# Optimization experiments

Hardware: AMD Instinct MI355X
Metric: run time of the kernel (lower is better)

The kernel has to match this reference:

```python
import jax, jax.numpy as jnp
import numpy as np

NBIT = 8
NSPLIT = 255.0  # 2**NBIT - 1


def _quantized_matmul(x, w_clean, eps):
    # Faithful port of quantization(): bit-slice x into NBIT binary planes, run a
    # noisy linear per plane with weight w + randn*|w|*0.1, and sum. The 8
    # sequential fc() calls are fused into one einsum over the bit axis.
    # x: (..., in); w_clean: (out, in); eps: (NBIT, out, in) standard normal.
    mn = jnp.min(x)
    mx = jnp.max(x)
    q = ((x - mn) / (mx - mn) * NSPLIT).astype(jnp.uint8).astype(jnp.int32)  # truncating cast as in torch
    quant_base = 2 ** jnp.arange(NBIT, dtype=jnp.int32)
    binary = ((q[..., None] & quant_base) != 0).astype(x.dtype)              # (..., in, NBIT)
    scaled = binary * (2.0 ** jnp.arange(NBIT)).astype(x.dtype)              # plane i scaled by 2**i
    w_noisy = w_clean[None] + eps * jnp.abs(w_clean)[None] * 0.1             # (NBIT, out, in)
    z = jnp.einsum('...ib,boi->...o', scaled, w_noisy)
    return z, mn, mx, w_noisy[-1]  # fc.weight after loop == last noisy weight


def _forward(node_embedding, edge_embedding, nbr_mask, cond1, cond2, eps1, eps2, bn_gamma, bn_beta):
    B, At, Nbr, Fe = edge_embedding.shape
    Fn = node_embedding.shape[-1]
    c1 = jnp.concatenate(
        [jnp.broadcast_to(node_embedding[:, :, None, :], (B, At, Nbr, Fn)), edge_embedding],
        axis=3)                                                              # (B, At, Nbr, Fn+Fe)
    # quantization + re_quantization through fc (re-quant uses last noisy fc.weight)
    z1, mn1, mx1, w_last = _quantized_matmul(c1, cond1[0], eps1)
    bias1 = jnp.sum(mn1 * w_last, axis=1)                                    # (H1,)
    h = jax.nn.relu(z1 / NSPLIT * (mx1 - mn1) + bias1)                       # (B, At, Nbr, H1)
    # quantization + re_quantization through fc_2 (re-quant uses conductance[1][-1])
    z2, mn2, mx2, _ = _quantized_matmul(h, cond2[0], eps2)
    bias2 = jnp.sum(mn2 * cond2[-1], axis=1)                                 # (2*Fn,)
    c2 = z2 / NSPLIT * (mx2 - mn2) + bias2                                   # (B, At, Nbr, 2*Fn)
    nbr_gate, nbr_extract = jnp.split(c2, 2, axis=3)
    nbr_sumed = jax.nn.sigmoid(nbr_gate) * jnp.tanh(nbr_extract) * nbr_mask[..., None]
    nbr_sumed = jnp.sum(nbr_sumed, axis=2)                                   # (B, At, Fn)
    # BatchNorm1d in training mode: batch statistics over flattened (B*At)
    flat = nbr_sumed.reshape(-1, Fn)
    mean = jnp.mean(flat, axis=0)
    var = jnp.var(flat, axis=0)  # biased variance, as torch BN uses for normalization
    bn = ((flat - mean) / jnp.sqrt(var + 1e-5) * bn_gamma + bn_beta).reshape(B, At, Fn)
    return jax.nn.relu(node_embedding + bn)


def setup_inputs() -> dict:
    key = jax.random.key(0)
    ks = jax.random.split(key, 7)
    B, At, Nbr, Fn, Fe = 16, 96, 12, 64, 64
    H1, H2 = 4 * (Fn + Fe), 2 * Fn
    return {
        'node_embedding': jax.random.normal(ks[0], (B, At, Fn), jnp.float32),
        'edge_embedding': jax.random.normal(ks[1], (B, At, Nbr, Fe), jnp.float32),
        'nbr_mask': (jax.random.uniform(ks[2], (B, At, Nbr)) > 0.5).astype(jnp.float32),
        'cond1': jax.random.normal(ks[3], (2, H1, Fn + Fe), jnp.float32) * 0.05,
        'cond2': jax.random.normal(ks[4], (2, H2, H1), jnp.float32) * 0.05,
        'eps1': jax.random.normal(ks[5], (NBIT, H1, Fn + Fe), jnp.float32),
        'eps2': jax.random.normal(ks[6], (NBIT, H2, H1), jnp.float32),
        'bn_gamma': jnp.ones((Fn,), jnp.float32),
        'bn_beta': jnp.zeros((Fn,), jnp.float32),
    }


def reference(node_embedding, edge_embedding, nbr_mask, cond1, cond2, eps1, eps2, bn_gamma, bn_beta):
    return _forward(node_embedding, edge_embedding, nbr_mask, cond1, cond2, eps1, eps2, bn_gamma, bn_beta)
```

## Files before the change

kernel.cpp:

```cpp
#include <hip/hip_runtime.h>
#include <stdint.h>

#define B_    16
#define AT_   96
#define NBR_  12
#define FN_   64
#define FE_   64
#define M1    (B_*AT_*NBR_)
#define R_    (B_*AT_)
#define K1Q   128
#define N1    512
#define K2Q   512
#define N2    128
#define SPLIT2 4

typedef _Float16 f16x8 __attribute__((ext_vector_type(8)));
typedef float    f32x4 __attribute__((ext_vector_type(4)));
typedef __attribute__((address_space(1))) const void gconst_void;
typedef __attribute__((address_space(3))) void lds_void;

#define OFF_SCAL  0u
#define OFF_Q1    256u
#define OFF_W1E   (OFF_Q1  + (size_t)M1*K1Q)
#define OFF_B1    (OFF_W1E + (size_t)N1*K1Q*8*2)
#define OFF_B2    (OFF_B1  + (size_t)N1*4)
#define OFF_W2E   (OFF_B2  + (size_t)N2*4 + 256)
#define OFF_Q2    (OFF_W2E + (size_t)N2*K2Q*8*2)
#define OFF_H     (OFF_Q2  + (size_t)M1*K2Q)
#define OFF_ZP    OFF_H
#define OFF_NS    (OFF_H   + (size_t)M1*N1*4)

__device__ __forceinline__ unsigned int enc_f(float f) {
    unsigned int u = __float_as_uint(f);
    return (u & 0x80000000u) ? ~u : (u | 0x80000000u);
}
__device__ __forceinline__ float dec_f(unsigned int u) {
    return __uint_as_float((u & 0x80000000u) ? (u & 0x7FFFFFFFu) : ~u);
}

__global__ void k_init(unsigned int* scal) {
    if (threadIdx.x == 0) {
        scal[0] = 0xFFFFFFFFu; scal[1] = 0u;
        scal[2] = 0xFFFFFFFFu; scal[3] = 0u;
    }
}

__global__ __launch_bounds__(256) void k_minmax_c1(const float* __restrict__ node,
                                                   const float* __restrict__ edge,
                                                   unsigned int* __restrict__ scal) {
    const int nn = B_*AT_*FN_;
    const int ntot = nn + M1*FE_;
    float mn = 3.0e38f, mx = -3.0e38f;
    for (int idx = blockIdx.x*blockDim.x + threadIdx.x; idx < ntot; idx += gridDim.x*blockDim.x) {
        float x = (idx < nn) ? node[idx] : edge[idx - nn];
        mn = fminf(mn, x); mx = fmaxf(mx, x);
    }
    __shared__ float smn[256], smx[256];
    smn[threadIdx.x] = mn; smx[threadIdx.x] = mx; __syncthreads();
    for (int s = 128; s > 0; s >>= 1) {
        if (threadIdx.x < s) {
            smn[threadIdx.x] = fminf(smn[threadIdx.x], smn[threadIdx.x+s]);
            smx[threadIdx.x] = fmaxf(smx[threadIdx.x], smx[threadIdx.x+s]);
        }
        __syncthreads();
    }
    if (threadIdx.x == 0) { atomicMin(&scal[0], enc_f(smn[0])); atomicMax(&scal[1], enc_f(smx[0])); }
}

template<int KQ, int N>
__global__ __launch_bounds__(256) void k_prep_w16(const float* __restrict__ w_clean,
                                                  const float* __restrict__ eps,
                                                  const unsigned int* __restrict__ scal, int sbase,
                                                  _Float16* __restrict__ We) {
    int idx = blockIdx.x*blockDim.x + threadIdx.x;
    if (idx >= N*KQ) return;
    int o = idx / KQ, i = idx % KQ;
    float mn = dec_f(scal[sbase]), mx = dec_f(scal[sbase+1]);
    float s = (mx - mn) * (1.0f/255.0f);
    float w = w_clean[idx];
    float aw = fabsf(w) * 0.1f;
    union { _Float16 h[8]; uint4 u; } pk;
    float p = s;
    #pragma unroll
    for (int b = 0; b < 8; b++) {
        float e = eps[(size_t)b*N*KQ + idx];
        pk.h[b] = (_Float16)((w + e*aw) * p);
        p *= 2.0f;
    }
    *(uint4*)&We[((size_t)o*KQ + i)*8] = pk.u;
}

__global__ void k_bias1(const float* __restrict__ cond1, const float* __restrict__ eps1,
                        const unsigned int* __restrict__ scal, float* __restrict__ bias1) {
    int o = blockIdx.x*blockDim.x + threadIdx.x;
    if (o >= N1) return;
    float mn = dec_f(scal[0]);
    float ssum = 0.f;
    for (int i = 0; i < K1Q; i++) {
        float w = cond1[o*K1Q + i];
        float e = eps1[7*(N1*K1Q) + o*K1Q + i];
        ssum += w + (e * fabsf(w)) * 0.1f;
    }
    bias1[o] = mn * ssum;
}

__global__ void k_bias2(const float* __restrict__ cond2, const unsigned int* __restrict__ scal,
                        float* __restrict__ bias2) {
    int o = blockIdx.x*blockDim.x + threadIdx.x;
    if (o >= N2) return;
    float mn = dec_f(scal[2]);
    const float* w2 = cond2 + N2*K2Q;
    float ssum = 0.f;
    for (int i = 0; i < K2Q; i++) ssum += w2[o*K2Q + i];
    bias2[o] = mn * ssum;
}

__global__ __launch_bounds__(256) void k_quant_c1(const float* __restrict__ node,
                                                  const float* __restrict__ edge,
                                                  const unsigned int* __restrict__ scal,
                                                  unsigned int* __restrict__ q1) {
    int idx = blockIdx.x*256 + threadIdx.x;
    int m = idx >> 5, dw = idx & 31;
    const float mn = dec_f(scal[0]), rng = dec_f(scal[1]) - mn;
    float4 x;
    if (dw < 16) x = *(const float4*)&node[(m/NBR_)*FN_ + dw*4];
    else         x = *(const float4*)&edge[(size_t)m*FE_ + (dw-16)*4];
    unsigned int b0 = (unsigned char)(int)((x.x - mn) / rng * 255.0f);
    unsigned int b1 = (unsigned char)(int)((x.y - mn) / rng * 255.0f);
    unsigned int b2 = (unsigned char)(int)((x.z - mn) / rng * 255.0f);
    unsigned int b3 = (unsigned char)(int)((x.w - mn) / rng * 255.0f);
    q1[idx] = b0 | (b1 << 8) | (b2 << 16) | (b3 << 24);
}

__global__ __launch_bounds__(256) void k_quant_h(const float* __restrict__ h,
                                                 const unsigned int* __restrict__ scal,
                                                 unsigned int* __restrict__ q2) {
    int idx = blockIdx.x*256 + threadIdx.x;
    const float mn = dec_f(scal[2]), rng = dec_f(scal[3]) - mn;
    float4 x = *(const float4*)&h[(size_t)idx*4];
    unsigned int b0 = (unsigned char)(int)((x.x - mn) / rng * 255.0f);
    unsigned int b1 = (unsigned char)(int)((x.y - mn) / rng * 255.0f);
    unsigned int b2 = (unsigned char)(int)((x.z - mn) / rng * 255.0f);
    unsigned int b3 = (unsigned char)(int)((x.w - mn) / rng * 255.0f);
    q2[idx] = b0 | (b1 << 8) | (b2 << 16) | (b3 << 24);
}

__device__ __forceinline__ f16x8 expand_byte(unsigned int byte) {
    unsigned int r2 = byte | (byte << 15);
    union { unsigned int u[4]; f16x8 h; } t;
    t.u[0] = ( r2       & 0x00010001u) * 0x3C00u;
    t.u[1] = ((r2 >> 2) & 0x00010001u) * 0x3C00u;
    t.u[2] = ((r2 >> 4) & 0x00010001u) * 0x3C00u;
    t.u[3] = ((r2 >> 6) & 0x00010001u) * 0x3C00u;
    return t.h;
}

template<int KQ, int N, int SPLITK, bool EPI1>
__global__ __launch_bounds__(256, 2) void k_gemm16(const unsigned char* __restrict__ q,
                                                   const _Float16* __restrict__ W,
                                                   const float* __restrict__ bias,
                                                   float* __restrict__ out,
                                                   unsigned int* __restrict__ scal) {
    constexpr int KP  = KQ * 8;
    constexpr int KPS = KP / SPLITK;
    __shared__ _Float16 Bs[128*64];
    __shared__ unsigned int Qs[256];

    const int tid  = threadIdx.x;
    const int lane = tid & 63;
    const int w    = tid >> 6;
    const int wm   = (w & 1) * 64;
    const int wn   = (w >> 1) * 64;
    const int l15  = lane & 15;
    const int lq   = lane >> 4;
    const int sh8  = lq * 8;
    const int m0   = blockIdx.x * 128;
    const int o0   = blockIdx.y * 128;
    const int kbase = blockIdx.z * KPS;

    f32x4 acc[4][4] = {};

    const size_t qrow = (size_t)(m0 + (tid >> 1)) * KQ + (tid & 1) * 4;

    #pragma unroll 1
    for (int it = 0; it < KPS/64; ++it) {
        const int kp0 = kbase + it*64;
        const int i0  = kp0 >> 3;
        __syncthreads();
        {
            unsigned int qa = *(const unsigned int*)(q + qrow + i0);
            #pragma unroll
            for (int iss = 0; iss < 4; ++iss) {
                int s   = iss*256 + tid;
                int n   = s >> 3;
                int csrc = (s & 7) ^ (n & 7);
                const _Float16* gp = W + (size_t)(o0 + n)*KP + kp0 + csrc*8;
                _Float16* lp = &Bs[(size_t)(iss*256 + (tid & ~63)) * 8];
                __builtin_amdgcn_global_load_lds((gconst_void*)gp, (lds_void*)lp, 16, 0, 0);
            }
            Qs[tid] = qa;
        }
        __builtin_amdgcn_s_waitcnt(0);
        __syncthreads();

        f16x8 bf[4][2];
        #pragma unroll
        for (int nf = 0; nf < 4; ++nf) {
            const int nl = wn + nf*16 + l15;
            #pragma unroll
            for (int kf = 0; kf < 2; ++kf) {
                const int ch = kf*4 + lq;
                bf[nf][kf] = *(const f16x8*)&Bs[nl*64 + ((ch ^ (nl & 7)) << 3)];
            }
        }
        #pragma unroll
        for (int mf = 0; mf < 4; ++mf) {
            uint2 qd = *(const uint2*)&Qs[(wm + mf*16 + l15) * 2];
            f16x8 a0 = expand_byte((qd.x >> sh8) & 0xFFu);
            f16x8 a1 = expand_byte((qd.y >> sh8) & 0xFFu);
            #pragma unroll
            for (int nf = 0; nf < 4; ++nf) {
                acc[mf][nf] = __builtin_amdgcn_mfma_f32_16x16x32_f16(a0, bf[nf][0], acc[mf][nf], 0, 0, 0);
                acc[mf][nf] = __builtin_amdgcn_mfma_f32_16x16x32_f16(a1, bf[nf][1], acc[mf][nf], 0, 0, 0);
            }
        }
    }

    if (EPI1) {
        float bv[4];
        #pragma unroll
        for (int nf = 0; nf < 4; ++nf) bv[nf] = bias[o0 + wn + nf*16 + l15];
        float tmn = 3.0e38f, tmx = -3.0e38f;
        #pragma unroll
        for (int mf = 0; mf < 4; ++mf) {
            const int mr = m0 + wm + mf*16 + lq*4;
            #pragma unroll
            for (int nf = 0; nf < 4; ++nf) {
                const int oc = o0 + wn + nf*16 + l15;
                #pragma unroll
                for (int r = 0; r < 4; ++r) {
                    float v = acc[mf][nf][r] + bv[nf];
                    v = fmaxf(v, 0.0f);
                    tmn = fminf(tmn, v); tmx = fmaxf(tmx, v);
                    out[(size_t)(mr + r)*N + oc] = v;
                }
            }
        }
        __syncthreads();
        float* red = (float*)Bs;
        red[tid] = tmn; red[256 + tid] = tmx;
        __syncthreads();
        for (int s = 128; s > 0; s >>= 1) {
            if (tid < s) {
                red[tid]       = fminf(red[tid],       red[tid + s]);
                red[256 + tid] = fmaxf(red[256 + tid], red[256 + tid + s]);
            }
            __syncthreads();
        }
        if (tid == 0) { atomicMin(&scal[2], enc_f(red[0])); atomicMax(&scal[3], enc_f(red[256])); }
    } else {
        float* op = out + (size_t)blockIdx.z * ((size_t)M1 * N);
        #pragma unroll
        for (int mf = 0; mf < 4; ++mf) {
            const int mr = m0 + wm + mf*16 + lq*4;
            #pragma unroll
            for (int nf = 0; nf < 4; ++nf) {
                const int oc = o0 + wn + nf*16 + l15;
                #pragma unroll
                for (int r = 0; r < 4; ++r)
                    op[(size_t)(mr + r)*N + oc] = acc[mf][nf][r];
            }
        }
    }
}

__global__ void k_nbr(const float* __restrict__ zp, const float* __restrict__ bias2,
                      const float* __restrict__ mask, float* __restrict__ ns) {
    const size_t SP = (size_t)M1 * N2;
    int r = blockIdx.x;
    int f = threadIdx.x;
    float bg = bias2[f], be = bias2[64 + f];
    float s = 0.f;
    #pragma unroll
    for (int n = 0; n < NBR_; n++) {
        int m = r*NBR_ + n;
        size_t base = (size_t)m * N2;
        float g = bg, e = be;
        #pragma unroll
        for (int z = 0; z < SPLIT2; z++) {
            g += zp[z*SP + base + f];
            e += zp[z*SP + base + 64 + f];
        }
        float sig = 1.0f / (1.0f + expf(-g));
        s += sig * tanhf(e) * mask[m];
    }
    ns[r*64 + f] = s;
}

__global__ __launch_bounds__(256) void k_bn(const float* __restrict__ ns,
                                            const float* __restrict__ node,
                                            const float* __restrict__ gamma,
                                            const float* __restrict__ beta,
                                            float* __restrict__ out) {
    int f = blockIdx.x;
    int tid = threadIdx.x;
    float x[6];
    float s = 0.f, ss = 0.f;
    #pragma unroll
    for (int k = 0; k < 6; k++) {
        int r = tid + k*256;
        x[k] = ns[r*64 + f];
        s += x[k]; ss += x[k]*x[k];
    }
    __shared__ float rs[256], rss[256];
    rs[tid] = s; rss[tid] = ss; __syncthreads();
    for (int st = 128; st > 0; st >>= 1) {
        if (tid < st) { rs[tid] += rs[tid+st]; rss[tid] += rss[tid+st]; }
        __syncthreads();
    }
    float mean = rs[0] / 1536.0f;
    float var  = rss[0] / 1536.0f - mean*mean;
    float denom = sqrtf(var + 1e-5f);
    float g = gamma[f], bt = beta[f];
    #pragma unroll
    for (int k = 0; k < 6; k++) {
        int r = tid + k*256;
        float v = node[r*64 + f] + ((x[k] - mean) / denom * g + bt);
        out[r*64 + f] = fmaxf(v, 0.f);
    }
}

extern "C" void kernel_launch(void* const* d_in, const int* in_sizes, int n_in,
                              void* d_out, int out_size, void* d_ws, size_t ws_size,
                              hipStream_t stream) {
    const float* node  = (const float*)d_in[0];
    const float* edge  = (const float*)d_in[1];
    const float* mask  = (const float*)d_in[2];
    const float* cond1 = (const float*)d_in[3];
    const float* cond2 = (const float*)d_in[4];
    const float* eps1  = (const float*)d_in[5];
    const float* eps2  = (const float*)d_in[6];
    const float* gamma = (const float*)d_in[7];
    const float* beta  = (const float*)d_in[8];
    float* out = (float*)d_out;
    char* ws = (char*)d_ws;

    unsigned int*  scal = (unsigned int*)(ws + OFF_SCAL);
    unsigned char* q1   = (unsigned char*)(ws + OFF_Q1);
    _Float16* W1e = (_Float16*)(ws + OFF_W1E);
    float*    b1  = (float*)(ws + OFF_B1);
    float*    b2  = (float*)(ws + OFF_B2);
    _Float16* W2e = (_Float16*)(ws + OFF_W2E);
    unsigned char* q2 = (unsigned char*)(ws + OFF_Q2);
    float* h  = (float*)(ws + OFF_H);
    float* zp = (float*)(ws + OFF_ZP);
    float* ns = (float*)(ws + OFF_NS);

    k_init<<<1, 64, 0, stream>>>(scal);
    k_minmax_c1<<<512, 256, 0, stream>>>(node, edge, scal);
    k_prep_w16<K1Q, N1><<<(N1*K1Q + 255)/256, 256, 0, stream>>>(cond1, eps1, scal, 0, W1e);
    k_bias1<<<(N1 + 63)/64, 64, 0, stream>>>(cond1, eps1, scal, b1);
    k_quant_c1<<<(M1*32)/256, 256, 0, stream>>>(node, edge, scal, (unsigned int*)q1);
    k_gemm16<K1Q, N1, 1, true><<<dim3(M1/128, N1/128, 1), 256, 0, stream>>>(q1, W1e, b1, h, scal);
    k_prep_w16<K2Q, N2><<<(N2*K2Q + 255)/256, 256, 0, stream>>>(cond2, eps2, scal, 2, W2e);
    k_bias2<<<(N2 + 63)/64, 64, 0, stream>>>(cond2, scal, b2);
    k_quant_h<<<(M1*128)/256, 256, 0, stream>>>(h, scal, (unsigned int*)q2);
    k_gemm16<K2Q, N2, SPLIT2, false><<<dim3(M1/128, N2/128, SPLIT2), 256, 0, stream>>>(q2, W2e, (const float*)nullptr, zp, scal);
    k_nbr<<<R_, 64, 0, stream>>>(zp, b2, mask, ns);
    k_bn<<<64, 256, 0, stream>>>(ns, node, gamma, beta, out);
}
```

Measured before the change: 212.1 us.

## Split GEMM tile along K across warps, fuse bias into weight prep, fp16 partials

```diff
diff --git a/kernel.cpp b/kernel.cpp
--- a/kernel.cpp
+++ b/kernel.cpp
@@ -20,11 +20,11 @@
 typedef __attribute__((address_space(3))) void lds_void;
 
 #define OFF_SCAL  0u
-#define OFF_Q1    256u
+#define OFF_B1R   256u
+#define OFF_B2R   (OFF_B1R + 2048u)
+#define OFF_Q1    4096u
 #define OFF_W1E   (OFF_Q1  + (size_t)M1*K1Q)
-#define OFF_B1    (OFF_W1E + (size_t)N1*K1Q*8*2)
-#define OFF_B2    (OFF_B1  + (size_t)N1*4)
-#define OFF_W2E   (OFF_B2  + (size_t)N2*4 + 256)
+#define OFF_W2E   (OFF_W1E + (size_t)N1*K1Q*8*2)
 #define OFF_Q2    (OFF_W2E + (size_t)N2*K2Q*8*2)
 #define OFF_H     (OFF_Q2  + (size_t)M1*K2Q)
 #define OFF_ZP    OFF_H
@@ -38,11 +38,11 @@
     return __uint_as_float((u & 0x80000000u) ? (u & 0x7FFFFFFFu) : ~u);
 }
 
-__global__ void k_init(unsigned int* scal) {
-    if (threadIdx.x == 0) {
-        scal[0] = 0xFFFFFFFFu; scal[1] = 0u;
-        scal[2] = 0xFFFFFFFFu; scal[3] = 0u;
-    }
+__global__ void k_init(unsigned int* scal, float* b1raw, float* b2raw) {
+    int t = threadIdx.x;
+    if (t == 0) { scal[0] = 0xFFFFFFFFu; scal[1] = 0u; scal[2] = 0xFFFFFFFFu; scal[3] = 0u; }
+    if (t < N1) b1raw[t] = 0.f;
+    if (t < N2) b2raw[t] = 0.f;
 }
 
 __global__ __launch_bounds__(256) void k_minmax_c1(const float* __restrict__ node,
@@ -67,52 +67,36 @@
     if (threadIdx.x == 0) { atomicMin(&scal[0], enc_f(smn[0])); atomicMax(&scal[1], enc_f(smx[0])); }
 }
 
-template<int KQ, int N>
+template<int KQ, int N, int SBASE, bool USE_SECOND>
 __global__ __launch_bounds__(256) void k_prep_w16(const float* __restrict__ w_clean,
                                                   const float* __restrict__ eps,
-                                                  const unsigned int* __restrict__ scal, int sbase,
+                                                  const unsigned int* __restrict__ scal,
+                                                  float* __restrict__ braw,
                                                   _Float16* __restrict__ We) {
     int idx = blockIdx.x*blockDim.x + threadIdx.x;
     if (idx >= N*KQ) return;
-    int o = idx / KQ, i = idx % KQ;
-    float mn = dec_f(scal[sbase]), mx = dec_f(scal[sbase+1]);
+    int o = idx / KQ;
+    int i = idx % KQ;
+    float mn = dec_f(scal[SBASE]), mx = dec_f(scal[SBASE+1]);
     float s = (mx - mn) * (1.0f/255.0f);
     float w = w_clean[idx];
     float aw = fabsf(w) * 0.1f;
     union { _Float16 h[8]; uint4 u; } pk;
     float p = s;
+    float v7 = 0.f;
     #pragma unroll
     for (int b = 0; b < 8; b++) {
         float e = eps[(size_t)b*N*KQ + idx];
-        pk.h[b] = (_Float16)((w + e*aw) * p);
+        float v = w + e*aw;
+        if (b == 7) v7 = v;
+        pk.h[b] = (_Float16)(v * p);
         p *= 2.0f;
     }
     *(uint4*)&We[((size_t)o*KQ + i)*8] = pk.u;
-}
-
-__global__ void k_bias1(const float* __restrict__ cond1, const float* __restrict__ eps1,
-                        const unsigned int* __restrict__ scal, float* __restrict__ bias1) {
-    int o = blockIdx.x*blockDim.x + threadIdx.x;
-    if (o >= N1) return;
-    float mn = dec_f(scal[0]);
-    float ssum = 0.f;
-    for (int i = 0; i < K1Q; i++) {
-        float w = cond1[o*K1Q + i];
-        float e = eps1[7*(N1*K1Q) + o*K1Q + i];
-        ssum += w + (e * fabsf(w)) * 0.1f;
-    }
-    bias1[o] = mn * ssum;
-}
-
-__global__ void k_bias2(const float* __restrict__ cond2, const unsigned int* __restrict__ scal,
-                        float* __restrict__ bias2) {
-    int o = blockIdx.x*blockDim.x + threadIdx.x;
-    if (o >= N2) return;
-    float mn = dec_f(scal[2]);
-    const float* w2 = cond2 + N2*K2Q;
-    float ssum = 0.f;
-    for (int i = 0; i < K2Q; i++) ssum += w2[o*K2Q + i];
-    bias2[o] = mn * ssum;
+    float bv = USE_SECOND ? w_clean[(size_t)N*KQ + idx] : v7;
+    #pragma unroll
+    for (int off = 32; off > 0; off >>= 1) bv += __shfl_down(bv, off);
+    if ((threadIdx.x & 63) == 0) atomicAdd(&braw[o], bv);
 }
 
 __global__ __launch_bounds__(256) void k_quant_c1(const float* __restrict__ node,
@@ -156,98 +140,118 @@
 }
 
 template<int KQ, int N, int SPLITK, bool EPI1>
-__global__ __launch_bounds__(256, 2) void k_gemm16(const unsigned char* __restrict__ q,
-                                                   const _Float16* __restrict__ W,
-                                                   const float* __restrict__ bias,
-                                                   float* __restrict__ out,
-                                                   unsigned int* __restrict__ scal) {
+__global__ __launch_bounds__(256, 4) void kg(const unsigned char* __restrict__ q,
+                                             const _Float16* __restrict__ W,
+                                             const float* __restrict__ braw,
+                                             void* __restrict__ outv,
+                                             unsigned int* __restrict__ scal) {
     constexpr int KP  = KQ * 8;
     constexpr int KPS = KP / SPLITK;
-    __shared__ _Float16 Bs[128*64];
-    __shared__ unsigned int Qs[256];
+    __shared__ _Float16 Bs[8192];
+    __shared__ uint2    Qs[256];
 
     const int tid  = threadIdx.x;
     const int lane = tid & 63;
     const int w    = tid >> 6;
     const int wm   = (w & 1) * 64;
-    const int wn   = (w >> 1) * 64;
+    const int kg   = w >> 1;
     const int l15  = lane & 15;
     const int lq   = lane >> 4;
     const int sh8  = lq * 8;
     const int m0   = blockIdx.x * 128;
-    const int o0   = blockIdx.y * 128;
+    const int o0   = blockIdx.y * 64;
     const int kbase = blockIdx.z * KPS;
 
     f32x4 acc[4][4] = {};
 
-    const size_t qrow = (size_t)(m0 + (tid >> 1)) * KQ + (tid & 1) * 4;
+    const int akg = tid >> 7, agt = tid & 127;
+    const unsigned char* aq = q + (size_t)(m0 + agt)*KQ + (kbase >> 3) + akg*64;
 
     #pragma unroll 1
-    for (int it = 0; it < KPS/64; ++it) {
-        const int kp0 = kbase + it*64;
-        const int i0  = kp0 >> 3;
-        __syncthreads();
-        {
-            unsigned int qa = *(const unsigned int*)(q + qrow + i0);
-            #pragma unroll
-            for (int iss = 0; iss < 4; ++iss) {
-                int s   = iss*256 + tid;
-                int n   = s >> 3;
-                int csrc = (s & 7) ^ (n & 7);
-                const _Float16* gp = W + (size_t)(o0 + n)*KP + kp0 + csrc*8;
-                _Float16* lp = &Bs[(size_t)(iss*256 + (tid & ~63)) * 8];
-                __builtin_amdgcn_global_load_lds((gconst_void*)gp, (lds_void*)lp, 16, 0, 0);
-            }
-            Qs[tid] = qa;
-        }
+    for (int it = 0; it < KPS/128; ++it) {
+        __syncthreads();
+        uint2 qa = *(const uint2*)(aq + it*8);
+        #pragma unroll
+        for (int iss = 0; iss < 4; ++iss) {
+            int s    = iss*256 + tid;
+            int skg  = s >> 9;
+            int sg   = s & 511;
+            int n    = sg >> 3;
+            int csrc = (sg & 7) ^ (n & 7);
+            const _Float16* gp = W + (size_t)(o0 + n)*KP + kbase + skg*512 + it*64 + csrc*8;
+            _Float16* lp = &Bs[(size_t)(iss*256 + (tid & ~63)) * 8];
+            __builtin_amdgcn_global_load_lds((gconst_void*)gp, (lds_void*)lp, 16, 0, 0);
+        }
+        Qs[(akg << 7) + agt] = qa;
         __builtin_amdgcn_s_waitcnt(0);
         __syncthreads();
 
-        f16x8 bf[4][2];
+        uint2 qd[4];
         #pragma unroll
-        for (int nf = 0; nf < 4; ++nf) {
-            const int nl = wn + nf*16 + l15;
-            #pragma unroll
-            for (int kf = 0; kf < 2; ++kf) {
+        for (int mf = 0; mf < 4; ++mf)
+            qd[mf] = Qs[kg*128 + wm + mf*16 + l15];
+        #pragma unroll
+        for (int kf = 0; kf < 2; ++kf) {
+            f16x8 bf[4];
+            #pragma unroll
+            for (int nf = 0; nf < 4; ++nf) {
+                const int nl = nf*16 + l15;
                 const int ch = kf*4 + lq;
-                bf[nf][kf] = *(const f16x8*)&Bs[nl*64 + ((ch ^ (nl & 7)) << 3)];
-            }
-        }
-        #pragma unroll
-        for (int mf = 0; mf < 4; ++mf) {
-            uint2 qd = *(const uint2*)&Qs[(wm + mf*16 + l15) * 2];
-            f16x8 a0 = expand_byte((qd.x >> sh8) & 0xFFu);
-            f16x8 a1 = expand_byte((qd.y >> sh8) & 0xFFu);
-            #pragma unroll
-            for (int nf = 0; nf < 4; ++nf) {
-                acc[mf][nf] = __builtin_amdgcn_mfma_f32_16x16x32_f16(a0, bf[nf][0], acc[mf][nf], 0, 0, 0);
-                acc[mf][nf] = __builtin_amdgcn_mfma_f32_16x16x32_f16(a1, bf[nf][1], acc[mf][nf], 0, 0, 0);
-            }
+                bf[nf] = *(const f16x8*)&Bs[kg*4096 + nl*64 + ((ch ^ (nl & 7)) << 3)];
+            }
+            #pragma unroll
+            for (int mf = 0; mf < 4; ++mf) {
+                unsigned int byte = ((kf ? qd[mf].y : qd[mf].x) >> sh8) & 0xFFu;
+                f16x8 a = expand_byte(byte);
+                #pragma unroll
+                for (int nf = 0; nf < 4; ++nf)
+                    acc[mf][nf] = __builtin_amdgcn_mfma_f32_16x16x32_f16(a, bf[nf], acc[mf][nf], 0, 0, 0);
+            }
+        }
+    }
+
+    float* red = (float*)Bs;
+    #pragma unroll
+    for (int nf = 0; nf < 4; ++nf) {
+        __syncthreads();
+        if (kg == 1) {
+            #pragma unroll
+            for (int mf = 0; mf < 4; ++mf)
+                *(f32x4*)&red[(w & 1)*1024 + mf*256 + lane*4] = acc[mf][nf];
+        }
+        __syncthreads();
+        if (kg == 0) {
+            #pragma unroll
+            for (int mf = 0; mf < 4; ++mf)
+                acc[mf][nf] += *(const f32x4*)&red[(w & 1)*1024 + mf*256 + lane*4];
         }
     }
 
     if (EPI1) {
-        float bv[4];
-        #pragma unroll
-        for (int nf = 0; nf < 4; ++nf) bv[nf] = bias[o0 + wn + nf*16 + l15];
         float tmn = 3.0e38f, tmx = -3.0e38f;
-        #pragma unroll
-        for (int mf = 0; mf < 4; ++mf) {
-            const int mr = m0 + wm + mf*16 + lq*4;
-            #pragma unroll
-            for (int nf = 0; nf < 4; ++nf) {
-                const int oc = o0 + wn + nf*16 + l15;
+        if (kg == 0) {
+            float* out = (float*)outv;
+            const float mn1 = dec_f(scal[0]);
+            float bv[4];
+            #pragma unroll
+            for (int nf = 0; nf < 4; ++nf) bv[nf] = mn1 * braw[o0 + nf*16 + l15];
+            #pragma unroll
+            for (int mf = 0; mf < 4; ++mf) {
+                const int mr = m0 + wm + mf*16 + lq*4;
                 #pragma unroll
-                for (int r = 0; r < 4; ++r) {
-                    float v = acc[mf][nf][r] + bv[nf];
-                    v = fmaxf(v, 0.0f);
-                    tmn = fminf(tmn, v); tmx = fmaxf(tmx, v);
-                    out[(size_t)(mr + r)*N + oc] = v;
+                for (int nf = 0; nf < 4; ++nf) {
+                    const int oc = o0 + nf*16 + l15;
+                    #pragma unroll
+                    for (int r = 0; r < 4; ++r) {
+                        float v = acc[mf][nf][r] + bv[nf];
+                        v = fmaxf(v, 0.0f);
+                        tmn = fminf(tmn, v); tmx = fmaxf(tmx, v);
+                        out[(size_t)(mr + r)*N + oc] = v;
+                    }
                 }
             }
         }
         __syncthreads();
-        float* red = (float*)Bs;
         red[tid] = tmn; red[256 + tid] = tmx;
         __syncthreads();
         for (int s = 128; s > 0; s >>= 1) {
@@ -259,27 +263,34 @@
         }
         if (tid == 0) { atomicMin(&scal[2], enc_f(red[0])); atomicMax(&scal[3], enc_f(red[256])); }
     } else {
-        float* op = out + (size_t)blockIdx.z * ((size_t)M1 * N);
-        #pragma unroll
-        for (int mf = 0; mf < 4; ++mf) {
-            const int mr = m0 + wm + mf*16 + lq*4;
-            #pragma unroll
-            for (int nf = 0; nf < 4; ++nf) {
-                const int oc = o0 + wn + nf*16 + l15;
+        if (kg == 0) {
+            _Float16* op = (_Float16*)outv + (size_t)blockIdx.z * ((size_t)M1 * N);
+            #pragma unroll
+            for (int mf = 0; mf < 4; ++mf) {
+                const int mr = m0 + wm + mf*16 + lq*4;
                 #pragma unroll
-                for (int r = 0; r < 4; ++r)
-                    op[(size_t)(mr + r)*N + oc] = acc[mf][nf][r];
-            }
-        }
-    }
-}
-
-__global__ void k_nbr(const float* __restrict__ zp, const float* __restrict__ bias2,
-                      const float* __restrict__ mask, float* __restrict__ ns) {
+                for (int nf = 0; nf < 4; ++nf) {
+                    const int oc = o0 + nf*16 + l15;
+                    #pragma unroll
+                    for (int r = 0; r < 4; ++r)
+                        op[(size_t)(mr + r)*N + oc] = (_Float16)acc[mf][nf][r];
+                }
+            }
+        }
+    }
+}
+
+__global__ __launch_bounds__(256) void k_nbr(const _Float16* __restrict__ zp,
+                                             const float* __restrict__ b2raw,
+                                             const unsigned int* __restrict__ scal,
+                                             const float* __restrict__ mask,
+                                             float* __restrict__ ns) {
     const size_t SP = (size_t)M1 * N2;
-    int r = blockIdx.x;
-    int f = threadIdx.x;
-    float bg = bias2[f], be = bias2[64 + f];
+    int tid = threadIdx.x;
+    int r = blockIdx.x*4 + (tid >> 6);
+    int f = tid & 63;
+    const float mn2 = dec_f(scal[2]);
+    float bg = mn2 * b2raw[f], be = mn2 * b2raw[64 + f];
     float s = 0.f;
     #pragma unroll
     for (int n = 0; n < NBR_; n++) {
@@ -288,8 +299,8 @@
         float g = bg, e = be;
         #pragma unroll
         for (int z = 0; z < SPLIT2; z++) {
-            g += zp[z*SP + base + f];
-            e += zp[z*SP + base + 64 + f];
+            g += (float)zp[z*SP + base + f];
+            e += (float)zp[z*SP + base + 64 + f];
         }
         float sig = 1.0f / (1.0f + expf(-g));
         s += sig * tanhf(e) * mask[m];
@@ -346,26 +357,24 @@
     char* ws = (char*)d_ws;
 
     unsigned int*  scal = (unsigned int*)(ws + OFF_SCAL);
-    unsigned char* q1   = (unsigned char*)(ws + OFF_Q1);
+    float* b1raw = (float*)(ws + OFF_B1R);
+    float* b2raw = (float*)(ws + OFF_B2R);
+    unsigned char* q1 = (unsigned char*)(ws + OFF_Q1);
     _Float16* W1e = (_Float16*)(ws + OFF_W1E);
-    float*    b1  = (float*)(ws + OFF_B1);
-    float*    b2  = (float*)(ws + OFF_B2);
     _Float16* W2e = (_Float16*)(ws + OFF_W2E);
     unsigned char* q2 = (unsigned char*)(ws + OFF_Q2);
-    float* h  = (float*)(ws + OFF_H);
-    float* zp = (float*)(ws + OFF_ZP);
-    float* ns = (float*)(ws + OFF_NS);
-
-    k_init<<<1, 64, 0, stream>>>(scal);
+    float*    h  = (float*)(ws + OFF_H);
+    _Float16* zp = (_Float16*)(ws + OFF_ZP);
+    float*    ns = (float*)(ws + OFF_NS);
+
+    k_init<<<1, 1024, 0, stream>>>(scal, b1raw, b2raw);
     k_minmax_c1<<<512, 256, 0, stream>>>(node, edge, scal);
-    k_prep_w16<K1Q, N1><<<(N1*K1Q + 255)/256, 256, 0, stream>>>(cond1, eps1, scal, 0, W1e);
-    k_bias1<<<(N1 + 63)/64, 64, 0, stream>>>(cond1, eps1, scal, b1);
+    k_prep_w16<K1Q, N1, 0, false><<<(N1*K1Q + 255)/256, 256, 0, stream>>>(cond1, eps1, scal, b1raw, W1e);
     k_quant_c1<<<(M1*32)/256, 256, 0, stream>>>(node, edge, scal, (unsigned int*)q1);
-    k_gemm16<K1Q, N1, 1, true><<<dim3(M1/128, N1/128, 1), 256, 0, stream>>>(q1, W1e, b1, h, scal);
-    k_prep_w16<K2Q, N2><<<(N2*K2Q + 255)/256, 256, 0, stream>>>(cond2, eps2, scal, 2, W2e);
-    k_bias2<<<(N2 + 63)/64, 64, 0, stream>>>(cond2, scal, b2);
+    kg<K1Q, N1, 1, true><<<dim3(M1/128, N1/64, 1), 256, 0, stream>>>(q1, W1e, b1raw, h, scal);
+    k_prep_w16<K2Q, N2, 2, true><<<(N2*K2Q + 255)/256, 256, 0, stream>>>(cond2, eps2, scal, b2raw, W2e);
     k_quant_h<<<(M1*128)/256, 256, 0, stream>>>(h, scal, (unsigned int*)q2);
-    k_gemm16<K2Q, N2, SPLIT2, false><<<dim3(M1/128, N2/128, SPLIT2), 256, 0, stream>>>(q2, W2e, (const float*)nullptr, zp, scal);
-    k_nbr<<<R_, 64, 0, stream>>>(zp, b2, mask, ns);
+    kg<K2Q, N2, SPLIT2, false><<<dim3(M1/128, N2/64, SPLIT2), 256, 0, stream>>>(q2, W2e, b2raw, zp, scal);
+    k_nbr<<<R_/4, 256, 0, stream>>>(zp, b2raw, scal, mask, ns);
     k_bn<<<64, 256, 0, stream>>>(ns, node, gamma, beta, out);
 }
```

Result: faster. 198.8 us (-6.3%).
